# Performance work log

Measured on AMD Instinct MI355X. Metric: run time of the kernel, lower is better.

Reference implementation:

```python
import jax, jax.numpy as jnp
import numpy as np

B, S, D = 4, 2048, 1024
H = 8  # hardcoded in AttentionLayer
HD = D // H
FF = 4096
EPS = 1e-5


def _layernorm(x):
    # LayerNorm(hidden_dim, elementwise_affine=False), eps=1e-5
    mu = jnp.mean(x, axis=-1, keepdims=True)
    var = jnp.var(x, axis=-1, keepdims=True)
    return (x - mu) / jnp.sqrt(var + EPS)


def setup_inputs() -> dict:
    key = jax.random.key(0)
    ks = jax.random.split(key, 5)
    scale = 0.02
    return {
        "x": jax.random.normal(ks[0], (B, S, D), dtype=jnp.float32),
        "qkv_proj": jax.random.normal(ks[1], (D, 3 * D), dtype=jnp.float32) * scale,
        "o_proj": jax.random.normal(ks[2], (D, D), dtype=jnp.float32) * scale,
        "ff1": jax.random.normal(ks[3], (D, FF), dtype=jnp.float32) * scale,
        "ff2": jax.random.normal(ks[4], (FF, D), dtype=jnp.float32) * scale,
    }


def reference(x, qkv_proj, o_proj, ff1, ff2):
    b, s, d = x.shape
    # --- attention ---
    qkv = jnp.matmul(x, qkv_proj)                       # [b,s,3d]
    qkv = qkv.reshape(b, s, H, 3 * HD).transpose(0, 2, 1, 3)  # [b,h,s,3hd]
    q, k, v = jnp.split(qkv, 3, axis=-1)                # each [b,h,s,hd]
    logits = jnp.einsum('bhqd,bhkd->bhqk', q, k) / jnp.sqrt(jnp.float32(HD))
    attn = jax.nn.softmax(logits, axis=-1)
    vals = jnp.einsum('bhqk,bhkd->bhqd', attn, v)       # [b,h,s,hd]
    vals = vals.transpose(0, 2, 1, 3).reshape(b, s, d)
    attn_out = jnp.matmul(vals, o_proj)
    # --- residual + norm + FFN + residual + norm ---
    x = _layernorm(x + attn_out)
    ff_out = jnp.matmul(jax.nn.relu(jnp.matmul(x, ff1)), ff2)
    x = _layernorm(x + ff_out)
    return x
```

## Files before the change

### kernel.cpp

```cpp
#include <hip/hip_runtime.h>
#include <hip/hip_bf16.h>


typedef float floatx4 __attribute__((ext_vector_type(4)));
typedef float floatx16 __attribute__((ext_vector_type(16)));
typedef short bf16x8 __attribute__((ext_vector_type(8)));

#define DEVI __device__ __forceinline__

typedef const __attribute__((address_space(1))) unsigned int* gas1_t;
typedef __attribute__((address_space(3))) unsigned int* las3_t;

DEVI void gll16(const void* g, void* l) {
  __builtin_amdgcn_global_load_lds((gas1_t)g, (las3_t)l, 16, 0, 0);
}

DEVI short bfbits(float f) {
  __hip_bfloat16 h = __float2bfloat16(f);
  return *reinterpret_cast<short*>(&h);
}

DEVI unsigned int cvtpk(float lo, float hi) {
  unsigned int r;
  asm("v_cvt_pk_bf16_f32 %0, %1, %2" : "=v"(r) : "v"(lo), "v"(hi));
  return r;
}

template<int EPI, int SPLITK>
__global__ __launch_bounds__(512, 2) void gemm256(
    const __hip_bfloat16* __restrict__ A,
    const __hip_bfloat16* __restrict__ BT,
    __hip_bfloat16* __restrict__ Cb, __hip_bfloat16* __restrict__ Cb2,
    int M, int N, int K)
{
  __shared__ __align__(16) char lds[131072];
  const int tid = threadIdx.x;
  const int wave = tid >> 6, lane = tid & 63;
  const int lane15 = lane & 15, quad = lane >> 4;
  const int wm = wave >> 2, wn = wave & 3;
  const int row0 = blockIdx.x * 256, col0 = blockIdx.y * 256;
  const int Kh = K / SPLITK;
  const size_t kofs = (SPLITK > 1) ? (size_t)blockIdx.z * Kh : 0;
  const int NT = Kh >> 6;

  floatx4 acc[8][4] = {};

  const int srow = tid >> 3;
  const int sblk = (tid & 7) ^ (srow & 7);
  const __hip_bfloat16* Ag = A + (size_t)(row0 + srow) * K + kofs + sblk * 8;
  const __hip_bfloat16* Bg = BT + (size_t)(col0 + srow) * K + kofs + sblk * 8;

  auto stA = [&](int h, int p, int kt, int bf_) {
    gll16(Ag + (size_t)(p * 128 + h * 64) * (size_t)K + (size_t)kt * 64,
          lds + ((h << 1) + bf_) * 16384 + p * 8192 + (tid << 4));
  };
  auto stB = [&](int h, int q, int kt, int bf_) {
    gll16(Bg + (size_t)(h * 128 + q * 64) * (size_t)K + (size_t)kt * 64,
          lds + 65536 + ((h << 1) + bf_) * 16384 + q * 8192 + (tid << 4));
  };

  const int x7 = lane15 & 7;
  const int ck0 = (quad ^ x7) << 4;
  const int ck1 = ((4 + quad) ^ x7) << 4;
  const int aoff = (wm * 64 + lane15) * 128;
  const int boff = ((wn & 1) * 64 + lane15) * 128;
  const int bhalf = wn >> 1;

  stA(0, 0, 0, 0); stA(0, 1, 0, 0);
  stA(1, 0, 0, 0); stA(1, 1, 0, 0);
  stB(0, 0, 0, 0); stB(0, 1, 0, 0); stB(1, 0, 0, 0); stB(1, 1, 0, 0);
  stA(0, 0, 1, 1); stA(0, 1, 1, 1);
  stB(0, 0, 1, 1); stB(0, 1, 1, 1); stB(1, 0, 1, 1); stB(1, 1, 1, 1);
  asm volatile("s_waitcnt vmcnt(6)" ::: "memory");
  asm volatile("s_barrier" ::: "memory");

  for (int t = 0; t < NT; ++t) {
    const int cb = t & 1, nb = cb ^ 1;
    const char* As0 = lds + cb * 16384 + aoff;
    const char* As1 = lds + (2 + cb) * 16384 + aoff;
    const char* Bs_ = lds + 65536 + ((bhalf << 1) + cb) * 16384 + boff;

    bf16x8 af[4][2], bq[4][2];
#pragma unroll
    for (int i = 0; i < 4; i++) {
      af[i][0] = *(const bf16x8*)(As0 + i * 2048 + ck0);
      af[i][1] = *(const bf16x8*)(As0 + i * 2048 + ck1);
    }
#pragma unroll
    for (int j = 0; j < 4; j++) {
      bq[j][0] = *(const bf16x8*)(Bs_ + j * 2048 + ck0);
      bq[j][1] = *(const bf16x8*)(Bs_ + j * 2048 + ck1);
    }
    if (t + 1 < NT) { stA(1, 0, t + 1, nb); stA(1, 1, t + 1, nb); }
    asm volatile("s_barrier" ::: "memory");
    __builtin_amdgcn_s_setprio(1);
#pragma unroll
    for (int i = 0; i < 4; i++)
#pragma unroll
      for (int j = 0; j < 4; j++) {
        acc[i][j] = __builtin_amdgcn_mfma_f32_16x16x32_bf16(af[i][0], bq[j][0], acc[i][j], 0, 0, 0);
        acc[i][j] = __builtin_amdgcn_mfma_f32_16x16x32_bf16(af[i][1], bq[j][1], acc[i][j], 0, 0, 0);
      }
    __builtin_amdgcn_s_setprio(0);
    asm volatile("s_barrier" ::: "memory");

#pragma unroll
    for (int i = 0; i < 4; i++) {
      af[i][0] = *(const bf16x8*)(As1 + i * 2048 + ck0);
      af[i][1] = *(const bf16x8*)(As1 + i * 2048 + ck1);
    }
    if (t + 2 < NT) {
      stA(0, 0, t + 2, cb); stA(0, 1, t + 2, cb);
      stB(0, 0, t + 2, cb); stB(0, 1, t + 2, cb);
      stB(1, 0, t + 2, cb); stB(1, 1, t + 2, cb);
      asm volatile("s_waitcnt vmcnt(6)" ::: "memory");
    } else if (t + 1 < NT) {
      asm volatile("s_waitcnt vmcnt(0)" ::: "memory");
    }
    asm volatile("s_barrier" ::: "memory");
    __builtin_amdgcn_s_setprio(1);
#pragma unroll
    for (int i = 0; i < 4; i++)
#pragma unroll
      for (int j = 0; j < 4; j++) {
        acc[4 + i][j] = __builtin_amdgcn_mfma_f32_16x16x32_bf16(af[i][0], bq[j][0], acc[4 + i][j], 0, 0, 0);
        acc[4 + i][j] = __builtin_amdgcn_mfma_f32_16x16x32_bf16(af[i][1], bq[j][1], acc[4 + i][j], 0, 0, 0);
      }
    __builtin_amdgcn_s_setprio(0);
    asm volatile("s_barrier" ::: "memory");
  }

  __hip_bfloat16* Cp = (SPLITK > 1 && blockIdx.z) ? Cb2 : Cb;
#pragma unroll
  for (int i = 0; i < 8; i++) {
    const int mb = row0 + wm * 128 + i * 16 + quad * 4;
#pragma unroll
    for (int j = 0; j < 4; j++) {
      const int n = col0 + wn * 64 + j * 16 + lane15;
      const float fac = (EPI == 0 && (((n >> 7) % 3) == 0)) ? 0.12751729f : 1.f;
#pragma unroll
      for (int r = 0; r < 4; r++) {
        const size_t idx = (size_t)(mb + r) * N + n;
        const float v = acc[i][j][r];
        if (EPI == 0) {
          Cb[idx] = __float2bfloat16(v * fac);
        } else if (EPI == 2) {
          Cb[idx] = __float2bfloat16(v > 0.f ? v : 0.f);
        } else {
          Cp[idx] = __float2bfloat16(v);
        }
      }
    }
  }
}

__global__ __launch_bounds__(256, 2) void attn_kernel(
    const __hip_bfloat16* __restrict__ qkv,
    const __hip_bfloat16* __restrict__ Vt,
    __hip_bfloat16* __restrict__ vals)
{
  __shared__ __hip_bfloat16 Ak[128 * 128];
  __shared__ __hip_bfloat16 Bq[128 * 128];

  const int tid = threadIdx.x;
  const int wave = tid >> 6, lane = tid & 63;
  const int l31 = lane & 31, l5 = lane >> 5;
  const int bh = blockIdx.x, qt = blockIdx.y;
  const int b = bh >> 3, h = bh & 7;
  const size_t tokbase = (size_t)b * 2048;

  const int sw8 = ((tid & 15) ^ (tid >> 4)) * 8;
  const int srow = tid >> 4;
  const int srowp = (srow & 3) | ((srow << 1) & 8) | ((srow >> 1) & 4);
  const __hip_bfloat16* qg  = qkv + (tokbase + qt * 128) * 3072 + h * 384 + sw8;
  const __hip_bfloat16* kg0 = qkv + tokbase * 3072 + h * 384 + 128 + sw8;
  const __hip_bfloat16* vg0 = Vt + (size_t)bh * 128 * 2048 + sw8;

#pragma unroll
  for (int rd = 0; rd < 8; rd++)
    gll16(qg + (size_t)(rd * 16 + srow) * 3072, (char*)Bq + rd * 4096 + tid * 16);
  __syncthreads();

  const int rx = l31 & 15;
  bf16x8 qf[8];
  {
    const char* qb = (const char*)Bq + (wave * 32 + l31) * 256;
#pragma unroll
    for (int ks = 0; ks < 8; ks++)
      qf[ks] = *(const bf16x8*)(qb + (((ks * 2 + l5) ^ rx) << 4));
  }
#pragma unroll
  for (int rd = 0; rd < 8; rd++)
    gll16(kg0 + (size_t)(rd * 16 + srowp) * 3072, (char*)Ak + rd * 4096 + tid * 16);
  __syncthreads();

  floatx16 oacc[4] = {};
  float lsum = 0.f;

  for (int kt = 0; kt < 16; kt++) {
    if (kt) __syncthreads();

#pragma unroll
    for (int rd = 0; rd < 8; rd++)
      gll16(vg0 + (size_t)kt * 128 + (size_t)(rd * 16 + srow) * 2048,
            (char*)Bq + rd * 4096 + tid * 16);

    floatx16 sacc[4] = {};
    __builtin_amdgcn_s_setprio(1);
#pragma unroll
    for (int ks = 0; ks < 8; ks++) {
      const int off = ((ks * 2 + l5) ^ rx) << 4;
      const char* kb = (const char*)Ak + l31 * 256 + off;
#pragma unroll
      for (int nt = 0; nt < 4; nt++) {
        const bf16x8 ak = *(const bf16x8*)(kb + nt * 8192);
        sacc[nt] = __builtin_amdgcn_mfma_f32_32x32x16_bf16(ak, qf[ks], sacc[nt], 0, 0, 0);
      }
    }
    __builtin_amdgcn_s_setprio(0);

    bf16x8 pf[8];
#pragma unroll
    for (int c = 0; c < 8; c++) {
      const int nt = c >> 1, bi = (c & 1) * 8;
      const float p0 = exp2f(sacc[nt][bi + 0]);
      const float p1 = exp2f(sacc[nt][bi + 1]);
      const float p2 = exp2f(sacc[nt][bi + 2]);
      const float p3 = exp2f(sacc[nt][bi + 3]);
      const float p4 = exp2f(sacc[nt][bi + 4]);
      const float p5 = exp2f(sacc[nt][bi + 5]);
      const float p6 = exp2f(sacc[nt][bi + 6]);
      const float p7 = exp2f(sacc[nt][bi + 7]);
      lsum += ((p0 + p1) + (p2 + p3)) + ((p4 + p5) + (p6 + p7));
      union { uint4 u; bf16x8 v; } w;
      w.u.x = cvtpk(p0, p1); w.u.y = cvtpk(p2, p3);
      w.u.z = cvtpk(p4, p5); w.u.w = cvtpk(p6, p7);
      pf[c] = w.v;
    }

    __syncthreads();
    if (kt < 15) {
#pragma unroll
      for (int rd = 0; rd < 8; rd++)
        gll16(kg0 + (size_t)((kt + 1) * 128 + rd * 16 + srowp) * 3072,
              (char*)Ak + rd * 4096 + tid * 16);
    }

    __builtin_amdgcn_s_setprio(1);
#pragma unroll
    for (int ks = 0; ks < 8; ks++) {
      const int off = ((ks * 2 + l5) ^ rx) << 4;
      const char* vb = (const char*)Bq + l31 * 256 + off;
#pragma unroll
      for (int nt = 0; nt < 4; nt++) {
        const bf16x8 av = *(const bf16x8*)(vb + nt * 8192);
        oacc[nt] = __builtin_amdgcn_mfma_f32_32x32x16_bf16(av, pf[ks], oacc[nt], 0, 0, 0);
      }
    }
    __builtin_amdgcn_s_setprio(0);
  }

  lsum += __shfl_xor(lsum, 32);
  const float linv = 1.f / lsum;

  const size_t row = tokbase + (size_t)qt * 128 + wave * 32 + l31;
  __hip_bfloat16* vrow = vals + row * 1024 + h * 128 + 4 * l5;
#pragma unroll
  for (int nt = 0; nt < 4; nt++)
#pragma unroll
    for (int g = 0; g < 4; g++) {
      uint2 pk;
      pk.x = cvtpk(oacc[nt][g * 4 + 0] * linv, oacc[nt][g * 4 + 1] * linv);
      pk.y = cvtpk(oacc[nt][g * 4 + 2] * linv, oacc[nt][g * 4 + 3] * linv);
      *(uint2*)(vrow + nt * 32 + g * 8) = pk;
    }
}

__global__ __launch_bounds__(256) void prep_k(
    const float* __restrict__ x, __hip_bfloat16* __restrict__ xb,
    const float* __restrict__ qkvw, __hip_bfloat16* __restrict__ qkvT,
    const float* __restrict__ ow, __hip_bfloat16* __restrict__ oT,
    const float* __restrict__ f1, __hip_bfloat16* __restrict__ f1T,
    const float* __restrict__ f2, __hip_bfloat16* __restrict__ f2T)
{
  const int bid = blockIdx.x;
  if (bid < 8192) {
    const size_t i = (size_t)bid * 256 + threadIdx.x;
    const float4 v = ((const float4*)x)[i];
    short4 sv;
    sv.x = bfbits(v.x); sv.y = bfbits(v.y); sv.z = bfbits(v.z); sv.w = bfbits(v.w);
    ((short4*)xb)[i] = sv;
    return;
  }
  int t = bid - 8192;
  const float* W; __hip_bfloat16* WT; int K, N, nbx;
  if (t < 3072) { W = qkvw; WT = qkvT; K = 1024; N = 3072; nbx = 96; }
  else if (t < 3072 + 1024) { t -= 3072; W = ow; WT = oT; K = 1024; N = 1024; nbx = 32; }
  else if (t < 3072 + 1024 + 4096) { t -= 3072 + 1024; W = f1; WT = f1T; K = 1024; N = 4096; nbx = 128; }
  else { t -= 3072 + 1024 + 4096; W = f2; WT = f2T; K = 4096; N = 1024; nbx = 32; }
  __shared__ float tl[32][33];
  const int tx = threadIdx.x & 31, ty = threadIdx.x >> 5;
  const int n0 = (t % nbx) * 32, k0 = (t / nbx) * 32;
#pragma unroll
  for (int i = 0; i < 4; i++)
    tl[ty + i * 8][tx] = W[(size_t)(k0 + ty + i * 8) * N + n0 + tx];
  __syncthreads();
#pragma unroll
  for (int i = 0; i < 4; i++)
    WT[(size_t)(n0 + ty + i * 8) * K + k0 + tx] = __float2bfloat16(tl[tx][ty + i * 8]);
}

__global__ __launch_bounds__(256) void vtrans_k(const __hip_bfloat16* __restrict__ qkv,
                                                __hip_bfloat16* __restrict__ Vt) {
  __shared__ __hip_bfloat16 t[32][33];
  const int tx = threadIdx.x & 31, ty = threadIdx.x >> 5;
  const int s0 = blockIdx.x * 32, d0 = blockIdx.y * 32, bh = blockIdx.z;
  const int b = bh >> 3, h = bh & 7;
#pragma unroll
  for (int i = 0; i < 4; i++)
    t[ty + i * 8][tx] = qkv[((size_t)b * 2048 + s0 + ty + i * 8) * 3072 + h * 384 + 256 + d0 + tx];
  __syncthreads();
#pragma unroll
  for (int i = 0; i < 4; i++)
    Vt[((size_t)bh * 128 + d0 + ty + i * 8) * 2048 + s0 + tx] = t[tx][ty + i * 8];
}

template<bool FINAL>
__global__ __launch_bounds__(256) void ln_red_k(
    const __hip_bfloat16* __restrict__ p0, const __hip_bfloat16* __restrict__ p1,
    const __hip_bfloat16* __restrict__ res,
    __hip_bfloat16* __restrict__ ob, float* __restrict__ of) {
  const int row = blockIdx.x, tid = threadIdx.x;
  const size_t base = (size_t)row * 1024;
  const short4 a4 = ((const short4*)(p0 + base))[tid];
  const short4 b4 = ((const short4*)(p1 + base))[tid];
  const short4 r4 = ((const short4*)(res + base))[tid];
#define BF(x) __bfloat162float(*(const __hip_bfloat16*)&(x))
  float4 v;
  v.x = BF(a4.x) + BF(b4.x) + BF(r4.x);
  v.y = BF(a4.y) + BF(b4.y) + BF(r4.y);
  v.z = BF(a4.z) + BF(b4.z) + BF(r4.z);
  v.w = BF(a4.w) + BF(b4.w) + BF(r4.w);
#undef BF
  float s = v.x + v.y + v.z + v.w;
  float q = v.x * v.x + v.y * v.y + v.z * v.z + v.w * v.w;
#pragma unroll
  for (int off = 32; off; off >>= 1) { s += __shfl_xor(s, off); q += __shfl_xor(q, off); }
  __shared__ float ss[4], sq[4];
  const int wave = tid >> 6;
  if ((tid & 63) == 0) { ss[wave] = s; sq[wave] = q; }
  __syncthreads();
  s = ss[0] + ss[1] + ss[2] + ss[3];
  q = sq[0] + sq[1] + sq[2] + sq[3];
  const float mean = s * (1.f / 1024.f);
  const float var = q * (1.f / 1024.f) - mean * mean;
  const float rstd = rsqrtf(var + 1e-5f);
  float4 o;
  o.x = (v.x - mean) * rstd; o.y = (v.y - mean) * rstd;
  o.z = (v.z - mean) * rstd; o.w = (v.w - mean) * rstd;
  if (FINAL) {
    ((float4*)(of + base))[tid] = o;
  } else {
    short4 sv;
    sv.x = bfbits(o.x); sv.y = bfbits(o.y); sv.z = bfbits(o.z); sv.w = bfbits(o.w);
    ((short4*)(ob + base))[tid] = sv;
  }
}

extern "C" void kernel_launch(void* const* d_in, const int* in_sizes, int n_in,
                              void* d_out, int out_size, void* d_ws, size_t ws_size,
                              hipStream_t stream) {
  const float* x    = (const float*)d_in[0];
  const float* qkvw = (const float*)d_in[1];
  const float* ow   = (const float*)d_in[2];
  const float* f1   = (const float*)d_in[3];
  const float* f2   = (const float*)d_in[4];
  float* out = (float*)d_out;

  char* ws = (char*)d_ws;
  const size_t MB = 1024 * 1024;
  __hip_bfloat16* xb   = (__hip_bfloat16*)(ws);
  __hip_bfloat16* vals = (__hip_bfloat16*)(ws + 16 * MB);
  __hip_bfloat16* P1f  = (__hip_bfloat16*)(ws + 16 * MB);
  __hip_bfloat16* qkvT = (__hip_bfloat16*)(ws + 32 * MB);
  __hip_bfloat16* oT   = (__hip_bfloat16*)(ws + 38 * MB);
  __hip_bfloat16* f1T  = (__hip_bfloat16*)(ws + 40 * MB);
  __hip_bfloat16* f2T  = (__hip_bfloat16*)(ws + 48 * MB);
  __hip_bfloat16* qkvb = (__hip_bfloat16*)(ws + 56 * MB);
  __hip_bfloat16* P0o  = (__hip_bfloat16*)(ws + 56 * MB);
  __hip_bfloat16* P1o  = (__hip_bfloat16*)(ws + 72 * MB);
  __hip_bfloat16* hmid = (__hip_bfloat16*)(ws + 56 * MB);
  __hip_bfloat16* Vt   = (__hip_bfloat16*)(ws + 104 * MB);
  __hip_bfloat16* x1b  = (__hip_bfloat16*)(ws + 120 * MB);
  __hip_bfloat16* P0f  = (__hip_bfloat16*)(ws + 136 * MB);
  (void)in_sizes; (void)n_in; (void)out_size; (void)ws_size;

  prep_k<<<20480, 256, 0, stream>>>(x, xb, qkvw, qkvT, ow, oT, f1, f1T, f2, f2T);
  gemm256<0, 1><<<dim3(32, 12, 1), 512, 0, stream>>>(xb, qkvT, qkvb, nullptr,
                                                     8192, 3072, 1024);
  vtrans_k<<<dim3(64, 4, 32), 256, 0, stream>>>(qkvb, Vt);
  attn_kernel<<<dim3(32, 16), 256, 0, stream>>>(qkvb, Vt, vals);
  gemm256<4, 2><<<dim3(32, 4, 2), 512, 0, stream>>>(vals, oT, P0o, P1o,
                                                    8192, 1024, 1024);
  ln_red_k<false><<<8192, 256, 0, stream>>>(P0o, P1o, xb, x1b, nullptr);
  gemm256<2, 1><<<dim3(32, 16, 1), 512, 0, stream>>>(x1b, f1T, hmid, nullptr,
                                                     8192, 4096, 1024);
  gemm256<4, 2><<<dim3(32, 4, 2), 512, 0, stream>>>(hmid, f2T, P0f, P1f,
                                                    8192, 1024, 4096);
  ln_red_k<true><<<8192, 256, 0, stream>>>(P0f, P1f, x1b, nullptr, out);
}
```

Before: 454.2 us.

## Reschedule GEMM barriers, drop attention setprio, and use perm-based bf16 packing

The GEMM main loop issues the next-tile A prefetch before the LDS fragment reads. It removes two of the four barriers per iteration and moves the second-half global loads ahead of the second MFMA block, so the wait lands after the compute. The attention kernel drops its s_setprio around the MFMA loops. The hardware v_cvt_pk_bf16_f32 is replaced by an add-0x8000 plus byte-perm rounding, which is round-half-up rather than round-to-nearest-even and handles NaN differently. With fewer barriers, LDS buffers could be overwritten by global_load_lds while other waves are still reading them.

After: 450.3 us. About the same (-0.9%).

```diff
diff --git a/kernel.cpp b/kernel.cpp
--- a/kernel.cpp
+++ b/kernel.cpp
@@ -20,10 +20,10 @@
   return *reinterpret_cast<short*>(&h);
 }
 
-DEVI unsigned int cvtpk(float lo, float hi) {
-  unsigned int r;
-  asm("v_cvt_pk_bf16_f32 %0, %1, %2" : "=v"(r) : "v"(lo), "v"(hi));
-  return r;
+DEVI unsigned int packbf(float lo, float hi) {
+  return __builtin_amdgcn_perm(__float_as_uint(hi) + 0x8000u,
+                               __float_as_uint(lo) + 0x8000u,
+                               0x07060302u);
 }
 
 template<int EPI, int SPLITK>
@@ -80,53 +80,53 @@
     const char* As1 = lds + (2 + cb) * 16384 + aoff;
     const char* Bs_ = lds + 65536 + ((bhalf << 1) + cb) * 16384 + boff;
 
-    bf16x8 af[4][2], bq[4][2];
+    if (t + 1 < NT) { stA(1, 0, t + 1, nb); stA(1, 1, t + 1, nb); }
+    bf16x8 af[8], bq[8];
 #pragma unroll
     for (int i = 0; i < 4; i++) {
-      af[i][0] = *(const bf16x8*)(As0 + i * 2048 + ck0);
-      af[i][1] = *(const bf16x8*)(As0 + i * 2048 + ck1);
+      af[2 * i]     = *(const bf16x8*)(As0 + i * 2048 + ck0);
+      af[2 * i + 1] = *(const bf16x8*)(As0 + i * 2048 + ck1);
     }
 #pragma unroll
     for (int j = 0; j < 4; j++) {
-      bq[j][0] = *(const bf16x8*)(Bs_ + j * 2048 + ck0);
-      bq[j][1] = *(const bf16x8*)(Bs_ + j * 2048 + ck1);
-    }
-    if (t + 1 < NT) { stA(1, 0, t + 1, nb); stA(1, 1, t + 1, nb); }
-    asm volatile("s_barrier" ::: "memory");
+      bq[2 * j]     = *(const bf16x8*)(Bs_ + j * 2048 + ck0);
+      bq[2 * j + 1] = *(const bf16x8*)(Bs_ + j * 2048 + ck1);
+    }
     __builtin_amdgcn_s_setprio(1);
 #pragma unroll
     for (int i = 0; i < 4; i++)
 #pragma unroll
       for (int j = 0; j < 4; j++) {
-        acc[i][j] = __builtin_amdgcn_mfma_f32_16x16x32_bf16(af[i][0], bq[j][0], acc[i][j], 0, 0, 0);
-        acc[i][j] = __builtin_amdgcn_mfma_f32_16x16x32_bf16(af[i][1], bq[j][1], acc[i][j], 0, 0, 0);
+        acc[i][j] = __builtin_amdgcn_mfma_f32_16x16x32_bf16(af[2 * i],     bq[2 * j],     acc[i][j], 0, 0, 0);
+        acc[i][j] = __builtin_amdgcn_mfma_f32_16x16x32_bf16(af[2 * i + 1], bq[2 * j + 1], acc[i][j], 0, 0, 0);
       }
     __builtin_amdgcn_s_setprio(0);
     asm volatile("s_barrier" ::: "memory");
 
-#pragma unroll
-    for (int i = 0; i < 4; i++) {
-      af[i][0] = *(const bf16x8*)(As1 + i * 2048 + ck0);
-      af[i][1] = *(const bf16x8*)(As1 + i * 2048 + ck1);
-    }
     if (t + 2 < NT) {
       stA(0, 0, t + 2, cb); stA(0, 1, t + 2, cb);
       stB(0, 0, t + 2, cb); stB(0, 1, t + 2, cb);
       stB(1, 0, t + 2, cb); stB(1, 1, t + 2, cb);
+    }
+#pragma unroll
+    for (int i = 0; i < 4; i++) {
+      af[2 * i]     = *(const bf16x8*)(As1 + i * 2048 + ck0);
+      af[2 * i + 1] = *(const bf16x8*)(As1 + i * 2048 + ck1);
+    }
+    __builtin_amdgcn_s_setprio(1);
+#pragma unroll
+    for (int i = 0; i < 4; i++)
+#pragma unroll
+      for (int j = 0; j < 4; j++) {
+        acc[4 + i][j] = __builtin_amdgcn_mfma_f32_16x16x32_bf16(af[2 * i],     bq[2 * j],     acc[4 + i][j], 0, 0, 0);
+        acc[4 + i][j] = __builtin_amdgcn_mfma_f32_16x16x32_bf16(af[2 * i + 1], bq[2 * j + 1], acc[4 + i][j], 0, 0, 0);
+      }
+    __builtin_amdgcn_s_setprio(0);
+    if (t + 2 < NT) {
       asm volatile("s_waitcnt vmcnt(6)" ::: "memory");
     } else if (t + 1 < NT) {
       asm volatile("s_waitcnt vmcnt(0)" ::: "memory");
     }
-    asm volatile("s_barrier" ::: "memory");
-    __builtin_amdgcn_s_setprio(1);
-#pragma unroll
-    for (int i = 0; i < 4; i++)
-#pragma unroll
-      for (int j = 0; j < 4; j++) {
-        acc[4 + i][j] = __builtin_amdgcn_mfma_f32_16x16x32_bf16(af[i][0], bq[j][0], acc[4 + i][j], 0, 0, 0);
-        acc[4 + i][j] = __builtin_amdgcn_mfma_f32_16x16x32_bf16(af[i][1], bq[j][1], acc[4 + i][j], 0, 0, 0);
-      }
-    __builtin_amdgcn_s_setprio(0);
     asm volatile("s_barrier" ::: "memory");
   }
 
@@ -206,7 +206,6 @@
             (char*)Bq + rd * 4096 + tid * 16);
 
     floatx16 sacc[4] = {};
-    __builtin_amdgcn_s_setprio(1);
 #pragma unroll
     for (int ks = 0; ks < 8; ks++) {
       const int off = ((ks * 2 + l5) ^ rx) << 4;
@@ -217,7 +216,6 @@
         sacc[nt] = __builtin_amdgcn_mfma_f32_32x32x16_bf16(ak, qf[ks], sacc[nt], 0, 0, 0);
       }
     }
-    __builtin_amdgcn_s_setprio(0);
 
     bf16x8 pf[8];
 #pragma unroll
@@ -233,8 +231,8 @@
       const float p7 = exp2f(sacc[nt][bi + 7]);
       lsum += ((p0 + p1) + (p2 + p3)) + ((p4 + p5) + (p6 + p7));
       union { uint4 u; bf16x8 v; } w;
-      w.u.x = cvtpk(p0, p1); w.u.y = cvtpk(p2, p3);
-      w.u.z = cvtpk(p4, p5); w.u.w = cvtpk(p6, p7);
+      w.u.x = packbf(p0, p1); w.u.y = packbf(p2, p3);
+      w.u.z = packbf(p4, p5); w.u.w = packbf(p6, p7);
       pf[c] = w.v;
     }
 
@@ -246,7 +244,6 @@
               (char*)Ak + rd * 4096 + tid * 16);
     }
 
-    __builtin_amdgcn_s_setprio(1);
 #pragma unroll
     for (int ks = 0; ks < 8; ks++) {
       const int off = ((ks * 2 + l5) ^ rx) << 4;
@@ -257,7 +254,6 @@
         oacc[nt] = __builtin_amdgcn_mfma_f32_32x32x16_bf16(av, pf[ks], oacc[nt], 0, 0, 0);
       }
     }
-    __builtin_amdgcn_s_setprio(0);
   }
 
   lsum += __shfl_xor(lsum, 32);
@@ -270,8 +266,8 @@
 #pragma unroll
     for (int g = 0; g < 4; g++) {
       uint2 pk;
-      pk.x = cvtpk(oacc[nt][g * 4 + 0] * linv, oacc[nt][g * 4 + 1] * linv);
-      pk.y = cvtpk(oacc[nt][g * 4 + 2] * linv, oacc[nt][g * 4 + 3] * linv);
+      pk.x = packbf(oacc[nt][g * 4 + 0] * linv, oacc[nt][g * 4 + 1] * linv);
+      pk.y = packbf(oacc[nt][g * 4 + 2] * linv, oacc[nt][g * 4 + 3] * linv);
       *(uint2*)(vrow + nt * 32 + g * 8) = pk;
     }
 }
```
